# Optimization experiments

Measured on AMD Instinct MI355X. Metric: run time of the kernel, lower is better.

The kernel has to match this reference:

```python
import jax, jax.numpy as jnp
import numpy as np

B, CN, T = 16, 22, 1000
EXP, FCH, SPD, NCLS = 300, 150, 100, 4
KS = (15, 75, 55)
_IU = np.triu_indices(SPD)
_VEC_SCALE = np.where(_IU[0] == _IU[1], 1.0, np.sqrt(2.0)).astype(np.float32)


def _ln(x, g, b, eps=1e-5):
    m = x.mean(-1, keepdims=True)
    v = x.var(-1, keepdims=True)
    return (x - m) / jnp.sqrt(v + eps) * g + b


def _block(x, w1, w2, w3, w4, g1, b1, w5, g2, b2):
    # x: (B, CN, T). Conv2d(1,1,(3,1), same) over electrode axis.
    h = jax.lax.conv_general_dilated(x[:, None], w1.reshape(1, 1, 3, 1), (1, 1),
                                     [(1, 1), (0, 0)],
                                     dimension_numbers=('NCHW', 'OIHW', 'NCHW'))[:, 0]
    # Conv2d(1, 300, (1,1)): pure channel broadcast-expand
    h = h[:, None, :, :] * w2[None, :, None, None]          # (B, EXP, CN, T)
    # Conv2dWithConstraint: depthwise spatial conv (groups=300) with max-norm=1 on each filter
    n = jnp.linalg.norm(w3, axis=1, keepdims=True)
    w3r = w3 * jnp.minimum(1.0, 1.0 / (n + 1e-12))
    h = jnp.einsum('bgct,gc->bgt', h, w3r)                  # height collapses -> (B, EXP, T)
    h = jnp.einsum('og,bgt->bot', w4, h)                    # pointwise -> (B, FCH, T)
    h = _ln(h, g1, b1)
    K = w5.shape[-1]
    # depthwise temporal conv, padding='same' (odd K)
    h = jax.lax.conv_general_dilated(h, w5, (1,), [(K // 2, K // 2)],
                                     dimension_numbers=('NCH', 'OIH', 'NCH'),
                                     feature_group_count=FCH)
    return _ln(h, g2, b2)


def setup_inputs():
    key = jax.random.key(0)
    ks = jax.random.split(key, 64)
    d = {'x': jax.random.normal(ks[0], (B, CN, T), jnp.float32)}
    i = 1
    for bi, K in zip((1, 2, 3), KS):
        d[f'b{bi}_w1'] = jax.random.normal(ks[i], (3,)) / np.sqrt(3); i += 1
        d[f'b{bi}_w2'] = jax.random.normal(ks[i], (EXP,)); i += 1
        d[f'b{bi}_w3'] = jax.random.normal(ks[i], (EXP, CN)) / np.sqrt(CN); i += 1
        d[f'b{bi}_w4'] = jax.random.normal(ks[i], (FCH, EXP)) / np.sqrt(EXP); i += 1
        d[f'b{bi}_g1'] = jnp.ones((T,)); d[f'b{bi}_b1'] = jnp.zeros((T,))
        d[f'b{bi}_w5'] = jax.random.normal(ks[i], (FCH, 1, K)) / np.sqrt(K); i += 1
        d[f'b{bi}_g2'] = jnp.ones((T,)); d[f'b{bi}_b2'] = jnp.zeros((T,))
    d['w_sconv'] = jax.random.normal(ks[i], (SPD, 3 * FCH)) / np.sqrt(3 * FCH); i += 1
    d['w_aff'] = jnp.eye(SPD) + 0.05 * jax.random.normal(ks[i], (SPD, SPD)); i += 1
    d['w_fc'] = jax.random.normal(ks[i], (NCLS, SPD * (SPD + 1) // 2)) / np.sqrt(SPD * (SPD + 1) // 2); i += 1
    d['b_fc'] = jnp.zeros((NCLS,))
    return d


def reference(x,
              b1_w1, b1_w2, b1_w3, b1_w4, b1_g1, b1_b1, b1_w5, b1_g2, b1_b2,
              b2_w1, b2_w2, b2_w3, b2_w4, b2_g1, b2_b1, b2_w5, b2_g2, b2_b2,
              b3_w1, b3_w2, b3_w3, b3_w4, b3_g1, b3_b1, b3_w5, b3_g2, b3_b2,
              w_sconv, w_aff, w_fc, b_fc):
    h1 = _block(x, b1_w1, b1_w2, b1_w3, b1_w4, b1_g1, b1_b1, b1_w5, b1_g2, b1_b2)
    h2 = _block(x, b2_w1, b2_w2, b2_w3, b2_w4, b2_g1, b2_b1, b2_w5, b2_g2, b2_b2)
    h3 = _block(x, b3_w1, b3_w2, b3_w3, b3_w4, b3_g1, b3_b1, b3_w5, b3_g2, b3_b2)
    h = jnp.concatenate([h1, h2, h3], axis=1)               # (B, 450, T)
    h = jnp.einsum('oi,bit->bot', w_sconv, h)               # (B, SPD, T)
    # PCOM: covariance pooling over time -> SPD matrix per sample
    xc = h - h.mean(-1, keepdims=True)
    cov = jnp.einsum('bit,bjt->bij', xc, xc) / (T - 1) + 1e-4 * jnp.eye(SPD)
    # AffineInvariantLayer: learnable congruence transform W P W^T
    P = jnp.einsum('ij,bjk,lk->bil', w_aff, cov, w_aff)
    # LogmLayer: matrix log via batched eigendecomposition
    w, v = jnp.linalg.eigh(P)
    L = jnp.einsum('bik,bk,bjk->bij', v, jnp.log(jnp.clip(w, 1e-6)), v)
    # Vec: upper-triangular half-vectorization (off-diag * sqrt(2)) -> 5050
    flat = L[:, _IU[0], _IU[1]] * _VEC_SCALE
    logits = flat @ w_fc.T + b_fc
    return (logits, flat)
```

## Files before the change

kernel.cpp:

```cpp
#include <hip/hip_runtime.h>

#define B_ 16
#define CN_ 22
#define T_ 1000
#define EXP_ 300
#define FCH_ 150
#define SPD_ 100
#define NSWEEP 8

typedef float v2f __attribute__((ext_vector_type(2)));

static constexpr unsigned long long OFF_M2   = 0ull;
static constexpr unsigned long long OFF_HCAT = 65536ull;
static constexpr unsigned long long OFF_XC   = OFF_HCAT + 28800000ull;
static constexpr unsigned long long OFF_COV  = OFF_XC   + 6400000ull;
static constexpr unsigned long long OFF_P    = OFF_COV  + 640000ull;
static constexpr unsigned long long OFF_G    = OFF_XC;

struct PrepPtrs  { const float* w1[3]; const float* w2[3]; const float* w3[3]; const float* w4[3]; };
struct FrontPtrs { const float* g1[3]; const float* b1[3]; const float* w5[3];
                   const float* g2[3]; const float* b2[3]; int K[3]; };

__device__ __forceinline__ float block_sum(float v, float* sbuf) {
  #pragma unroll
  for (int off = 32; off > 0; off >>= 1) v += __shfl_down(v, off, 64);
  const int wid  = threadIdx.x >> 6;
  const int lane = threadIdx.x & 63;
  const int nw   = blockDim.x >> 6;
  if (lane == 0) sbuf[wid] = v;
  __syncthreads();
  float r = 0.f;
  for (int w = 0; w < nw; ++w) r += sbuf[w];
  __syncthreads();
  return r;
}

__device__ __forceinline__ float dpp_shr1(float old_, float src) {
  return __builtin_bit_cast(float, __builtin_amdgcn_update_dpp(
      __builtin_bit_cast(int, old_), __builtin_bit_cast(int, src),
      0x138, 0xf, 0xf, false));
}
__device__ __forceinline__ float dpp_shl1(float old_, float src) {
  return __builtin_bit_cast(float, __builtin_amdgcn_update_dpp(
      __builtin_bit_cast(int, old_), __builtin_bit_cast(int, src),
      0x130, 0xf, 0xf, false));
}

__global__ __launch_bounds__(256) void k_prep(PrepPtrs pp, float* __restrict__ M2) {
  const int beta = blockIdx.x;
  __shared__ float w3r[EXP_*CN_];
  __shared__ float M[FCH_*CN_];
  const float* w1 = pp.w1[beta];
  const float* w2 = pp.w2[beta];
  const float* w3 = pp.w3[beta];
  const float* w4 = pp.w4[beta];

  for (int g = threadIdx.x; g < EXP_; g += 256) {
    float s = 0.f;
    for (int c = 0; c < CN_; ++c) { float w = w3[g*CN_ + c]; s += w*w; }
    float n = sqrtf(s);
    float scale = fminf(1.f, 1.f/(n + 1e-12f)) * w2[g];
    for (int c = 0; c < CN_; ++c) w3r[g*CN_ + c] = w3[g*CN_ + c] * scale;
  }
  __syncthreads();
  for (int idx = threadIdx.x; idx < FCH_*CN_; idx += 256) {
    int o = idx / CN_, c = idx - o*CN_;
    float acc = 0.f;
    for (int g = 0; g < EXP_; ++g) acc += w4[o*EXP_ + g] * w3r[g*CN_ + c];
    M[idx] = acc;
  }
  __syncthreads();
  const float k0 = w1[0], k1 = w1[1], k2 = w1[2];
  for (int idx = threadIdx.x; idx < FCH_*CN_; idx += 256) {
    int c = idx % CN_;
    float v = k1 * M[idx];
    if (c > 0)       v += k2 * M[idx - 1];
    if (c < CN_ - 1) v += k0 * M[idx + 1];
    M2[beta*FCH_*CN_ + idx] = v;
  }
}

__global__ __launch_bounds__(256) void k_front(const float* __restrict__ x,
                                               const float* __restrict__ M2,
                                               FrontPtrs fp,
                                               float* __restrict__ hcat) {
  const int wg   = blockIdx.x;
  const int beta = wg / (B_*FCH_);
  const int rem  = wg - beta*(B_*FCH_);
  const int b    = rem / FCH_;
  const int o    = rem - b*FCH_;
  const int K    = fp.K[beta];
  const int Kh   = K >> 1;

  __shared__ float m2[CN_];
  __shared__ float hb2[T_];
  __shared__ float w5s[80];
  __shared__ float red[8];

  if (threadIdx.x < CN_) m2[threadIdx.x] = M2[(beta*FCH_ + o)*CN_ + threadIdx.x];
  if (threadIdx.x < K)   w5s[threadIdx.x] = fp.w5[beta][o*K + threadIdx.x];
  __syncthreads();

  const float* xb = x + (size_t)b*CN_*T_;
  float hv[4];
  float psum = 0.f;
  #pragma unroll
  for (int e = 0; e < 4; ++e) {
    int t = threadIdx.x + 256*e;
    float acc = 0.f;
    if (t < T_) {
      #pragma unroll
      for (int c = 0; c < CN_; ++c) acc += m2[c] * xb[c*T_ + t];
    }
    hv[e] = acc; psum += acc;
  }
  float mean = block_sum(psum, red) * (1.f/T_);
  float pv = 0.f;
  #pragma unroll
  for (int e = 0; e < 4; ++e) { int t = threadIdx.x + 256*e; if (t < T_) { float d = hv[e]-mean; pv += d*d; } }
  float var = block_sum(pv, red) * (1.f/T_);
  float inv = rsqrtf(var + 1e-5f);
  const float* g1 = fp.g1[beta]; const float* b1 = fp.b1[beta];
  #pragma unroll
  for (int e = 0; e < 4; ++e) { int t = threadIdx.x + 256*e; if (t < T_) hb2[t] = (hv[e]-mean)*inv*g1[t] + b1[t]; }
  __syncthreads();

  float cv[4];
  float ps2 = 0.f;
  #pragma unroll
  for (int e = 0; e < 4; ++e) {
    int t = threadIdx.x + 256*e;
    float acc = 0.f;
    if (t < T_) {
      int lo = t - Kh;
      for (int k = 0; k < K; ++k) {
        int tt = lo + k;
        float hvv = (tt >= 0 && tt < T_) ? hb2[tt] : 0.f;
        acc += hvv * w5s[k];
      }
    }
    cv[e] = acc; ps2 += acc;
  }
  float mean2 = block_sum(ps2, red) * (1.f/T_);
  float pv2 = 0.f;
  #pragma unroll
  for (int e = 0; e < 4; ++e) { int t = threadIdx.x + 256*e; if (t < T_) { float d = cv[e]-mean2; pv2 += d*d; } }
  float var2 = block_sum(pv2, red) * (1.f/T_);
  float inv2 = rsqrtf(var2 + 1e-5f);
  const float* g2 = fp.g2[beta]; const float* b2 = fp.b2[beta];
  float* hrow = hcat + ((size_t)b*(3*FCH_) + beta*FCH_ + o)*T_;
  #pragma unroll
  for (int e = 0; e < 4; ++e) { int t = threadIdx.x + 256*e; if (t < T_) hrow[t] = (cv[e]-mean2)*inv2*g2[t] + b2[t]; }
}

__global__ __launch_bounds__(256) void k_sconv(const float* __restrict__ hcat,
                                               const float* __restrict__ wsc,
                                               float* __restrict__ xc) {
  const int b  = blockIdx.x / 10;
  const int s0 = (blockIdx.x % 10) * 10;
  __shared__ float ws[10*450];
  __shared__ float red[8];
  for (int idx = threadIdx.x; idx < 4500; idx += 256) {
    int s = idx / 450, i = idx - s*450;
    ws[idx] = wsc[(s0+s)*450 + i];
  }
  __syncthreads();
  float acc[10][4];
  #pragma unroll
  for (int s = 0; s < 10; ++s)
    #pragma unroll
    for (int e = 0; e < 4; ++e) acc[s][e] = 0.f;
  const float* hb = hcat + (size_t)b*450*T_;
  for (int i = 0; i < 450; ++i) {
    float xv[4];
    #pragma unroll
    for (int e = 0; e < 4; ++e) { int t = threadIdx.x + 256*e; xv[e] = (t < T_) ? hb[(size_t)i*T_ + t] : 0.f; }
    #pragma unroll
    for (int s = 0; s < 10; ++s) {
      float w = ws[s*450 + i];
      #pragma unroll
      for (int e = 0; e < 4; ++e) acc[s][e] += w * xv[e];
    }
  }
  for (int s = 0; s < 10; ++s) {
    float mu = block_sum(acc[s][0]+acc[s][1]+acc[s][2]+acc[s][3], red) * (1.f/T_);
    float* xr = xc + ((size_t)b*SPD_ + s0 + s)*T_;
    #pragma unroll
    for (int e = 0; e < 4; ++e) { int t = threadIdx.x + 256*e; if (t < T_) xr[t] = acc[s][e] - mu; }
  }
}

__global__ __launch_bounds__(256) void k_cov(const float* __restrict__ xc, float* __restrict__ cov) {
  const int b  = blockIdx.x / 5;
  const int j0 = (blockIdx.x % 5) * 20;
  __shared__ __align__(16) float xst[SPD_*100];
  const int it = threadIdx.x / 10;
  const int jj = threadIdx.x - it*10;
  const bool act = threadIdx.x < 250;
  double a64[4][2] = {{0.0,0.0},{0.0,0.0},{0.0,0.0},{0.0,0.0}};
  for (int ch = 0; ch < 10; ++ch) {
    __syncthreads();
    const int tc0 = ch*100;
    for (int idx = threadIdx.x; idx < SPD_*100; idx += 256) {
      int row = idx / 100, tt = idx - row*100;
      xst[idx] = xc[((size_t)b*SPD_ + row)*T_ + tc0 + tt];
    }
    __syncthreads();
    if (act) {
      float a32[4][2] = {{0,0},{0,0},{0,0},{0,0}};
      for (int t4 = 0; t4 < 100; t4 += 4) {
        float4 xi[4], xj[2];
        #pragma unroll
        for (int r = 0; r < 4; ++r) xi[r] = *(const float4*)&xst[(it + 25*r)*100 + t4];
        #pragma unroll
        for (int s = 0; s < 2; ++s) xj[s] = *(const float4*)&xst[(j0 + jj + 10*s)*100 + t4];
        #pragma unroll
        for (int r = 0; r < 4; ++r)
          #pragma unroll
          for (int s = 0; s < 2; ++s)
            a32[r][s] += xi[r].x*xj[s].x + xi[r].y*xj[s].y + xi[r].z*xj[s].z + xi[r].w*xj[s].w;
      }
      #pragma unroll
      for (int r = 0; r < 4; ++r)
        #pragma unroll
        for (int s = 0; s < 2; ++s) a64[r][s] += (double)a32[r][s];
    }
  }
  if (act) {
    #pragma unroll
    for (int r = 0; r < 4; ++r) {
      #pragma unroll
      for (int s = 0; s < 2; ++s) {
        int i = it + 25*r, j = j0 + jj + 10*s;
        double v = a64[r][s] * (1.0/999.0);
        if (i == j) v += 1e-4;
        cov[(size_t)b*SPD_*SPD_ + i*SPD_ + j] = (float)v;
      }
    }
  }
}

__global__ __launch_bounds__(256) void k_aff(const float* __restrict__ cov,
                                             const float* __restrict__ waff,
                                             float* __restrict__ P) {
  const int b  = blockIdx.x / 5;
  const int j0 = (blockIdx.x % 5) * 20;
  __shared__ float Cs[SPD_*101];
  __shared__ float Ws[20*100];
  __shared__ float T1s[100*20];
  for (int idx = threadIdx.x; idx < SPD_*SPD_; idx += 256) {
    int r = idx / 100, c = idx - r*100;
    Cs[r*101 + c] = cov[(size_t)b*SPD_*SPD_ + idx];
  }
  for (int idx = threadIdx.x; idx < 2000; idx += 256) {
    int jl = idx / 100, k = idx - jl*100;
    Ws[idx] = waff[(j0+jl)*100 + k];
  }
  __syncthreads();
  const int it = threadIdx.x / 10, jj = threadIdx.x % 10;
  const bool act = threadIdx.x < 250;
  if (act) {
    double acc[4][2] = {{0.0,0.0},{0.0,0.0},{0.0,0.0},{0.0,0.0}};
    for (int k = 0; k < 100; ++k) {
      double cvv[4], wv[2];
      #pragma unroll
      for (int r = 0; r < 4; ++r) cvv[r] = (double)Cs[(it + 25*r)*101 + k];
      #pragma unroll
      for (int s = 0; s < 2; ++s) wv[s] = (double)Ws[(jj + 10*s)*100 + k];
      #pragma unroll
      for (int r = 0; r < 4; ++r)
        #pragma unroll
        for (int s = 0; s < 2; ++s) acc[r][s] += cvv[r]*wv[s];
    }
    #pragma unroll
    for (int r = 0; r < 4; ++r)
      #pragma unroll
      for (int s = 0; s < 2; ++s)
        T1s[(it + 25*r)*20 + (jj + 10*s)] = (float)acc[r][s];
  }
  __syncthreads();
  if (act) {
    double acc[4][2] = {{0.0,0.0},{0.0,0.0},{0.0,0.0},{0.0,0.0}};
    for (int k = 0; k < 100; ++k) {
      double wv[4], tv[2];
      #pragma unroll
      for (int r = 0; r < 4; ++r) wv[r] = (double)waff[(it + 25*r)*100 + k];
      #pragma unroll
      for (int s = 0; s < 2; ++s) tv[s] = (double)T1s[k*20 + jj + 10*s];
      #pragma unroll
      for (int r = 0; r < 4; ++r)
        #pragma unroll
        for (int s = 0; s < 2; ++s) acc[r][s] += wv[r]*tv[s];
    }
    #pragma unroll
    for (int r = 0; r < 4; ++r)
      #pragma unroll
      for (int s = 0; s < 2; ++s)
        P[(size_t)b*SPD_*SPD_ + (it + 25*r)*100 + (j0 + jj + 10*s)] = (float)acc[r][s];
  }
}

__global__ __launch_bounds__(256)
__attribute__((amdgpu_waves_per_eu(1, 1)))
void k_eig(const float* __restrict__ P, float* __restrict__ Gout) {
  __shared__ __align__(16) float gbuf[2][256];
  __shared__ __align__(16) float nbuf[512];
  const int tid = threadIdx.x;
  const int b   = blockIdx.x;
  const int w   = tid >> 6;
  const int j   = tid & 63;
  const bool act = (j < 50);
  const int rb  = 25 * w;

  v2f A2[12], B2[12];
  float As, Bs;
  const float* Pb = P + (size_t)b*SPD_*SPD_;
  #pragma unroll
  for (int i = 0; i < 12; ++i) {
    A2[i].x = act ? Pb[(rb+2*i  )*SPD_ + j]      : 0.f;
    A2[i].y = act ? Pb[(rb+2*i+1)*SPD_ + j]      : 0.f;
    B2[i].x = act ? Pb[(rb+2*i  )*SPD_ + (99-j)] : 0.f;
    B2[i].y = act ? Pb[(rb+2*i+1)*SPD_ + (99-j)] : 0.f;
  }
  As = act ? Pb[(rb+24)*SPD_ + j]      : 0.f;
  Bs = act ? Pb[(rb+24)*SPD_ + (99-j)] : 0.f;

  {
    v2f pA2 = {0.f, 0.f}, pB2 = {0.f, 0.f};
    #pragma unroll
    for (int i = 0; i < 12; ++i) { pA2 += A2[i]*A2[i]; pB2 += B2[i]*B2[i]; }
    nbuf[j*8 + w*2 + 0] = pA2.x + pA2.y + As*As;
    nbuf[j*8 + w*2 + 1] = pB2.x + pB2.y + Bs*Bs;
  }
  __syncthreads();
  float nA, nB;
  {
    float4 u0 = *(const float4*)&nbuf[j*8];
    float4 u1 = *(const float4*)&nbuf[j*8+4];
    nA = (u0.x + u0.z) + (u1.x + u1.z);
    nB = (u0.y + u0.w) + (u1.y + u1.w);
  }
  float pg;
  {
    v2f pg2 = {0.f, 0.f};
    #pragma unroll
    for (int i = 0; i < 12; ++i) pg2 += A2[i]*B2[i];
    pg = pg2.x + pg2.y + As*Bs;
  }

  int par = 0;
  for (int sweep = 0; sweep < NSWEEP; ++sweep) {
    for (int r = 0; r < 99; ++r) {
      gbuf[par][j*4 + w] = pg;
      __syncthreads();
      float4 gp = *(const float4*)&gbuf[par][j*4];
      float gamma = (gp.x + gp.y) + (gp.z + gp.w);

      float g2v = gamma*gamma;
      float ab = nA*nB;
      float tau = (g2v > 1e-12f*ab) ? ((nB - nA) / (2.f*gamma)) : 1e30f;
      float t  = ((tau >= 0.f) ? 1.f : -1.f) / (fabsf(tau) + sqrtf(1.f + tau*tau));
      float cr = rsqrtf(1.f + t*t);
      float sr = t*cr;
      nA = nA - t*gamma;
      nB = nB + t*gamma;

      {
        float sendN = (j == 0) ? nB : nA;
        float rNA = dpp_shr1(nA, sendN);
        float rNB = dpp_shl1(nB, nB);
        float newB = (j == 49) ? nA : rNB;
        nA = rNA; nB = newB;
      }

      const v2f cr2 = {cr, cr};
      const v2f sr2 = {sr, sr};
      v2f na[12], nb[12], sa[12], rA[12], rB[12];
      float nas, nbs, sas, rAs, rBs;

      #pragma unroll
      for (int i = 0; i < 12; ++i) {
        na[i] = cr2*A2[i] - sr2*B2[i];
        nb[i] = sr2*A2[i] + cr2*B2[i];
      }
      nas = cr*As - sr*Bs;
      nbs = sr*As + cr*Bs;

      #pragma unroll
      for (int i = 0; i < 12; ++i) {
        sa[i].x = (j == 0) ? nb[i].x : na[i].x;
        sa[i].y = (j == 0) ? nb[i].y : na[i].y;
      }
      sas = (j == 0) ? nbs : nas;

      #pragma unroll
      for (int i = 0; i < 12; ++i) {
        rA[i].x = dpp_shr1(na[i].x, sa[i].x);
        rA[i].y = dpp_shr1(na[i].y, sa[i].y);
        rB[i].x = dpp_shl1(nb[i].x, nb[i].x);
        rB[i].y = dpp_shl1(nb[i].y, nb[i].y);
      }
      rAs = dpp_shr1(nas, sas);
      rBs = dpp_shl1(nbs, nbs);

      v2f pg2 = {0.f, 0.f};
      #pragma unroll
      for (int i = 0; i < 12; ++i) {
        A2[i] = rA[i];
        B2[i].x = (j == 49) ? na[i].x : rB[i].x;
        B2[i].y = (j == 49) ? na[i].y : rB[i].y;
        pg2 += A2[i]*B2[i];
      }
      As = rAs;
      Bs = (j == 49) ? nas : rBs;
      pg = pg2.x + pg2.y + As*Bs;
      par ^= 1;
    }
  }

  if (act) {
    float* Gb = Gout + (size_t)b*SPD_*SPD_;
    #pragma unroll
    for (int i = 0; i < 12; ++i) {
      Gb[j*SPD_ + rb + 2*i]   = A2[i].x;
      Gb[j*SPD_ + rb + 2*i+1] = A2[i].y;
      Gb[(50 + j)*SPD_ + rb + 2*i]   = B2[i].x;
      Gb[(50 + j)*SPD_ + rb + 2*i+1] = B2[i].y;
    }
    Gb[j*SPD_ + rb + 24]        = As;
    Gb[(50 + j)*SPD_ + rb + 24] = Bs;
  }
}

__global__ __launch_bounds__(256) void k_lout(const float* __restrict__ Gin,
                                              const float* __restrict__ wfc,
                                              const float* __restrict__ bfc,
                                              float* __restrict__ out) {
  __shared__ __align__(16) float G[SPD_*SPD_];
  __shared__ float wcs[SPD_];
  __shared__ float red[8];
  const int tid = threadIdx.x;
  const int b   = blockIdx.x;
  for (int idx = tid; idx < SPD_*SPD_; idx += 256)
    G[idx] = Gin[(size_t)b*SPD_*SPD_ + idx];
  __syncthreads();
  if (tid < SPD_) {
    const float* col = &G[tid*SPD_];
    double s = 0.0;
    for (int i = 0; i < SPD_; ++i) { double v = (double)col[i]; s += v*v; }
    double lam = sqrt(s);
    double lc  = (lam < 1e-6) ? 1e-6 : lam;
    wcs[tid] = (float)(log(lc) / ((s > 1e-300) ? s : 1e-300));
  }
  __syncthreads();

  float a0 = 0.f, a1 = 0.f, a2 = 0.f, a3 = 0.f;
  for (int tile = tid; tile < 625; tile += 256) {
    const int ti = (tile / 25) * 4;
    const int tj = (tile % 25) * 4;
    float acc[4][4];
    #pragma unroll
    for (int r = 0; r < 4; ++r)
      #pragma unroll
      for (int s = 0; s < 4; ++s) acc[r][s] = 0.f;
    for (int c = 0; c < SPD_; ++c) {
      const float* col = &G[c*SPD_];
      float4 ga = *(const float4*)&col[ti];
      float4 gb = *(const float4*)&col[tj];
      float wcv = wcs[c];
      float wa[4] = { wcv*ga.x, wcv*ga.y, wcv*ga.z, wcv*ga.w };
      float bv[4] = { gb.x, gb.y, gb.z, gb.w };
      #pragma unroll
      for (int r = 0; r < 4; ++r)
        #pragma unroll
        for (int s = 0; s < 4; ++s) acc[r][s] += wa[r]*bv[s];
    }
    const float RT2 = 1.41421356237309505f;
    #pragma unroll
    for (int r = 0; r < 4; ++r) {
      #pragma unroll
      for (int s = 0; s < 4; ++s) {
        int i = ti + r, jx = tj + s;
        if (i <= jx) {
          int idx = i*SPD_ - (i*(i+1))/2 + jx;
          float val = acc[r][s] * (i == jx ? 1.f : RT2);
          out[64 + b*5050 + idx] = val;
          a0 += val * wfc[idx];
          a1 += val * wfc[5050 + idx];
          a2 += val * wfc[10100 + idx];
          a3 += val * wfc[15150 + idx];
        }
      }
    }
  }
  a0 = block_sum(a0, red);
  a1 = block_sum(a1, red);
  a2 = block_sum(a2, red);
  a3 = block_sum(a3, red);
  if (tid == 0) {
    out[b*4 + 0] = a0 + bfc[0];
    out[b*4 + 1] = a1 + bfc[1];
    out[b*4 + 2] = a2 + bfc[2];
    out[b*4 + 3] = a3 + bfc[3];
  }
}

extern "C" void kernel_launch(void* const* d_in, const int* in_sizes, int n_in,
                              void* d_out, int out_size, void* d_ws, size_t ws_size,
                              hipStream_t stream) {
  (void)in_sizes; (void)n_in; (void)out_size; (void)ws_size;
  const float* x = (const float*)d_in[0];
  const float* bw[3][9];
  for (int i = 0; i < 3; ++i)
    for (int jx = 0; jx < 9; ++jx)
      bw[i][jx] = (const float*)d_in[1 + i*9 + jx];
  const float* w_sconv = (const float*)d_in[28];
  const float* w_aff   = (const float*)d_in[29];
  const float* w_fc    = (const float*)d_in[30];
  const float* b_fc    = (const float*)d_in[31];

  char* ws = (char*)d_ws;
  float*  M2   = (float*)(ws + OFF_M2);
  float*  hcat = (float*)(ws + OFF_HCAT);
  float*  xc   = (float*)(ws + OFF_XC);
  float*  cov  = (float*)(ws + OFF_COV);
  float*  P    = (float*)(ws + OFF_P);
  float*  G    = (float*)(ws + OFF_G);
  float*  out  = (float*)d_out;

  PrepPtrs pp; FrontPtrs fp;
  for (int i = 0; i < 3; ++i) {
    pp.w1[i] = bw[i][0]; pp.w2[i] = bw[i][1]; pp.w3[i] = bw[i][2]; pp.w4[i] = bw[i][3];
    fp.g1[i] = bw[i][4]; fp.b1[i] = bw[i][5]; fp.w5[i] = bw[i][6];
    fp.g2[i] = bw[i][7]; fp.b2[i] = bw[i][8];
  }
  fp.K[0] = 15; fp.K[1] = 75; fp.K[2] = 55;

  hipLaunchKernelGGL(k_prep,  dim3(3),            dim3(256), 0, stream, pp, M2);
  hipLaunchKernelGGL(k_front, dim3(3*B_*FCH_),    dim3(256), 0, stream, x, M2, fp, hcat);
  hipLaunchKernelGGL(k_sconv, dim3(B_*10),        dim3(256), 0, stream, hcat, w_sconv, xc);
  hipLaunchKernelGGL(k_cov,   dim3(B_*5),         dim3(256), 0, stream, xc, cov);
  hipLaunchKernelGGL(k_aff,   dim3(B_*5),         dim3(256), 0, stream, cov, w_aff, P);
  hipLaunchKernelGGL(k_eig,   dim3(B_),           dim3(256), 0, stream, P, G);
  hipLaunchKernelGGL(k_lout,  dim3(B_),           dim3(256), 0, stream, G, w_fc, b_fc, out);
}
```

Measured before the change: 1.087 ms.

## Run Jacobi eigensolver with two waves per matrix instead of four

The one-sided Jacobi kernel now splits each 100-row matrix across 2 wavefronts of 50 rows each instead of 4 of 25. Each thread holds twice as many register values, and the rotation loop is processed in chunks of five to limit live temporaries. The aim is a cheaper per-rotation cross-wave reduction and barrier, since only two partial dot products are combined through shared memory. In exchange each wave does twice the serial arithmetic per rotation and register pressure rises.

Result: slower. 1.293 ms (+19.0%).

```diff
diff --git a/kernel.cpp b/kernel.cpp
--- a/kernel.cpp
+++ b/kernel.cpp
@@ -300,61 +300,57 @@
   }
 }
 
-__global__ __launch_bounds__(256)
+__global__ __launch_bounds__(128)
 __attribute__((amdgpu_waves_per_eu(1, 1)))
 void k_eig(const float* __restrict__ P, float* __restrict__ Gout) {
-  __shared__ __align__(16) float gbuf[2][256];
-  __shared__ __align__(16) float nbuf[512];
+  __shared__ __align__(16) float gbuf[2][128];
+  __shared__ __align__(16) float nbuf[256];
   const int tid = threadIdx.x;
   const int b   = blockIdx.x;
   const int w   = tid >> 6;
   const int j   = tid & 63;
   const bool act = (j < 50);
-  const int rb  = 25 * w;
-
-  v2f A2[12], B2[12];
-  float As, Bs;
+  const int rb  = 50 * w;
+
+  v2f A2[25], B2[25];
   const float* Pb = P + (size_t)b*SPD_*SPD_;
   #pragma unroll
-  for (int i = 0; i < 12; ++i) {
+  for (int i = 0; i < 25; ++i) {
     A2[i].x = act ? Pb[(rb+2*i  )*SPD_ + j]      : 0.f;
     A2[i].y = act ? Pb[(rb+2*i+1)*SPD_ + j]      : 0.f;
     B2[i].x = act ? Pb[(rb+2*i  )*SPD_ + (99-j)] : 0.f;
     B2[i].y = act ? Pb[(rb+2*i+1)*SPD_ + (99-j)] : 0.f;
   }
-  As = act ? Pb[(rb+24)*SPD_ + j]      : 0.f;
-  Bs = act ? Pb[(rb+24)*SPD_ + (99-j)] : 0.f;
 
   {
     v2f pA2 = {0.f, 0.f}, pB2 = {0.f, 0.f};
     #pragma unroll
-    for (int i = 0; i < 12; ++i) { pA2 += A2[i]*A2[i]; pB2 += B2[i]*B2[i]; }
-    nbuf[j*8 + w*2 + 0] = pA2.x + pA2.y + As*As;
-    nbuf[j*8 + w*2 + 1] = pB2.x + pB2.y + Bs*Bs;
+    for (int i = 0; i < 25; ++i) { pA2 += A2[i]*A2[i]; pB2 += B2[i]*B2[i]; }
+    nbuf[j*4 + w*2 + 0] = pA2.x + pA2.y;
+    nbuf[j*4 + w*2 + 1] = pB2.x + pB2.y;
   }
   __syncthreads();
   float nA, nB;
   {
-    float4 u0 = *(const float4*)&nbuf[j*8];
-    float4 u1 = *(const float4*)&nbuf[j*8+4];
-    nA = (u0.x + u0.z) + (u1.x + u1.z);
-    nB = (u0.y + u0.w) + (u1.y + u1.w);
+    float4 u = *(const float4*)&nbuf[j*4];
+    nA = u.x + u.z;
+    nB = u.y + u.w;
   }
   float pg;
   {
     v2f pg2 = {0.f, 0.f};
     #pragma unroll
-    for (int i = 0; i < 12; ++i) pg2 += A2[i]*B2[i];
-    pg = pg2.x + pg2.y + As*Bs;
+    for (int i = 0; i < 25; ++i) pg2 += A2[i]*B2[i];
+    pg = pg2.x + pg2.y;
   }
 
   int par = 0;
   for (int sweep = 0; sweep < NSWEEP; ++sweep) {
     for (int r = 0; r < 99; ++r) {
-      gbuf[par][j*4 + w] = pg;
+      gbuf[par][j*2 + w] = pg;
       __syncthreads();
-      float4 gp = *(const float4*)&gbuf[par][j*4];
-      float gamma = (gp.x + gp.y) + (gp.z + gp.w);
+      v2f gp = *(const v2f*)&gbuf[par][j*2];
+      float gamma = gp.x + gp.y;
 
       float g2v = gamma*gamma;
       float ab = nA*nB;
@@ -375,45 +371,37 @@
 
       const v2f cr2 = {cr, cr};
       const v2f sr2 = {sr, sr};
-      v2f na[12], nb[12], sa[12], rA[12], rB[12];
-      float nas, nbs, sas, rAs, rBs;
-
-      #pragma unroll
-      for (int i = 0; i < 12; ++i) {
-        na[i] = cr2*A2[i] - sr2*B2[i];
-        nb[i] = sr2*A2[i] + cr2*B2[i];
+      v2f pg2 = {0.f, 0.f};
+      #pragma unroll
+      for (int c = 0; c < 5; ++c) {
+        const int base = c*5;
+        v2f na[5], nb[5], sa[5], rA[5], rB[5];
+        #pragma unroll
+        for (int i = 0; i < 5; ++i) {
+          na[i] = cr2*A2[base+i] - sr2*B2[base+i];
+          nb[i] = sr2*A2[base+i] + cr2*B2[base+i];
+        }
+        #pragma unroll
+        for (int i = 0; i < 5; ++i) {
+          sa[i].x = (j == 0) ? nb[i].x : na[i].x;
+          sa[i].y = (j == 0) ? nb[i].y : na[i].y;
+        }
+        #pragma unroll
+        for (int i = 0; i < 5; ++i) {
+          rA[i].x = dpp_shr1(na[i].x, sa[i].x);
+          rA[i].y = dpp_shr1(na[i].y, sa[i].y);
+          rB[i].x = dpp_shl1(nb[i].x, nb[i].x);
+          rB[i].y = dpp_shl1(nb[i].y, nb[i].y);
+        }
+        #pragma unroll
+        for (int i = 0; i < 5; ++i) {
+          A2[base+i] = rA[i];
+          B2[base+i].x = (j == 49) ? na[i].x : rB[i].x;
+          B2[base+i].y = (j == 49) ? na[i].y : rB[i].y;
+          pg2 += A2[base+i]*B2[base+i];
+        }
       }
-      nas = cr*As - sr*Bs;
-      nbs = sr*As + cr*Bs;
-
-      #pragma unroll
-      for (int i = 0; i < 12; ++i) {
-        sa[i].x = (j == 0) ? nb[i].x : na[i].x;
-        sa[i].y = (j == 0) ? nb[i].y : na[i].y;
-      }
-      sas = (j == 0) ? nbs : nas;
-
-      #pragma unroll
-      for (int i = 0; i < 12; ++i) {
-        rA[i].x = dpp_shr1(na[i].x, sa[i].x);
-        rA[i].y = dpp_shr1(na[i].y, sa[i].y);
-        rB[i].x = dpp_shl1(nb[i].x, nb[i].x);
-        rB[i].y = dpp_shl1(nb[i].y, nb[i].y);
-      }
-      rAs = dpp_shr1(nas, sas);
-      rBs = dpp_shl1(nbs, nbs);
-
-      v2f pg2 = {0.f, 0.f};
-      #pragma unroll
-      for (int i = 0; i < 12; ++i) {
-        A2[i] = rA[i];
-        B2[i].x = (j == 49) ? na[i].x : rB[i].x;
-        B2[i].y = (j == 49) ? na[i].y : rB[i].y;
-        pg2 += A2[i]*B2[i];
-      }
-      As = rAs;
-      Bs = (j == 49) ? nas : rBs;
-      pg = pg2.x + pg2.y + As*Bs;
+      pg = pg2.x + pg2.y;
       par ^= 1;
     }
   }
@@ -421,14 +409,12 @@
   if (act) {
     float* Gb = Gout + (size_t)b*SPD_*SPD_;
     #pragma unroll
-    for (int i = 0; i < 12; ++i) {
+    for (int i = 0; i < 25; ++i) {
       Gb[j*SPD_ + rb + 2*i]   = A2[i].x;
       Gb[j*SPD_ + rb + 2*i+1] = A2[i].y;
       Gb[(50 + j)*SPD_ + rb + 2*i]   = B2[i].x;
       Gb[(50 + j)*SPD_ + rb + 2*i+1] = B2[i].y;
     }
-    Gb[j*SPD_ + rb + 24]        = As;
-    Gb[(50 + j)*SPD_ + rb + 24] = Bs;
   }
 }
 
@@ -541,6 +527,6 @@
   hipLaunchKernelGGL(k_sconv, dim3(B_*10),        dim3(256), 0, stream, hcat, w_sconv, xc);
   hipLaunchKernelGGL(k_cov,   dim3(B_*5),         dim3(256), 0, stream, xc, cov);
   hipLaunchKernelGGL(k_aff,   dim3(B_*5),         dim3(256), 0, stream, cov, w_aff, P);
-  hipLaunchKernelGGL(k_eig,   dim3(B_),           dim3(256), 0, stream, P, G);
+  hipLaunchKernelGGL(k_eig,   dim3(B_),           dim3(128), 0, stream, P, G);
   hipLaunchKernelGGL(k_lout,  dim3(B_),           dim3(256), 0, stream, G, w_fc, b_fc, out);
 }
```
